# Optimization experiments

Measured on AMD Instinct MI355X. Metric: run time of the kernel, lower is better.

Reference implementation:

```python
import jax, jax.numpy as jnp
import numpy as np

C = 256
NH, NL, NP_ = 8, 3, 4
HD = C // NH
NLAYERS = 6


def sine_pos(H, W, num_feats=128, temperature=10000.0, eps=1e-6):
    # mmdet SinePositionalEncoding with normalize=True and an all-zero padding mask:
    # cumsum of ones -> (i+1), normalized by last element (H or W) * 2*pi.
    scale = 2.0 * np.pi
    y = (jnp.arange(1, H + 1, dtype=jnp.float32) / (H + eps)) * scale
    x = (jnp.arange(1, W + 1, dtype=jnp.float32) / (W + eps)) * scale
    d = jnp.arange(num_feats, dtype=jnp.float32)
    dim_t = temperature ** (2.0 * jnp.floor(d / 2.0) / num_feats)

    def interleave(p):  # p: (n, num_feats) -> sin on even dims, cos on odd dims, interleaved
        return jnp.stack([jnp.sin(p[:, 0::2]), jnp.cos(p[:, 1::2])], axis=-1).reshape(p.shape[0], -1)

    py = interleave(y[:, None] / dim_t)  # (H, num_feats)
    px = interleave(x[:, None] / dim_t)  # (W, num_feats)
    pos = jnp.concatenate([jnp.broadcast_to(py[:, None, :], (H, W, num_feats)),
                           jnp.broadcast_to(px[None, :, :], (H, W, num_feats))], axis=-1)
    return pos.reshape(H * W, 2 * num_feats)


def ref_points(H, W):
    # normalized pixel centers, (x, y) order, shape (H*W, 2)
    ry = (jnp.arange(H, dtype=jnp.float32) + 0.5) / H
    rx = (jnp.arange(W, dtype=jnp.float32) + 0.5) / W
    gy, gx = jnp.meshgrid(ry, rx, indexing='ij')
    return jnp.stack([gx.ravel(), gy.ravel()], axis=-1)


def ln(x, w, b, eps=1e-5):
    m = x.mean(-1, keepdims=True)
    v = x.var(-1, keepdims=True)
    return (x - m) / jnp.sqrt(v + eps) * w + b


def gnorm(x, w, b, groups=32, eps=1e-5):
    B, Ch, H, W = x.shape
    xg = x.reshape(B, groups, Ch // groups, H, W)
    m = xg.mean((2, 3, 4), keepdims=True)
    v = xg.var((2, 3, 4), keepdims=True)
    xg = (xg - m) / jnp.sqrt(v + eps)
    return xg.reshape(B, Ch, H, W) * w[None, :, None, None] + b[None, :, None, None]


def conv3x3(x, w):
    return jax.lax.conv_general_dilated(x, w, (1, 1), 'SAME',
                                        dimension_numbers=('NCHW', 'OIHW', 'NCHW'))


def ms_deform(value, shapes, loc, aw):
    # value (B,S,NH,HD); loc (B,L,NH,NL,NP,2) normalized [0,1]; aw (B,L,NH,NL,NP)
    # Matches F.grid_sample(..., align_corners=False, padding_mode='zeros').
    B, S, nH, hd = value.shape
    Lq, nP = loc.shape[1], loc.shape[4]
    out = jnp.zeros((B, Lq, nH, hd), value.dtype)
    start = 0
    for lvl, (H, W) in enumerate(shapes):
        v = value[:, start:start + H * W].transpose(0, 2, 1, 3)  # (B,nH,HW,hd)
        start += H * W
        l = loc[:, :, :, lvl]                 # (B,Lq,nH,nP,2)
        px = l[..., 0] * W - 0.5
        py = l[..., 1] * H - 0.5
        x0 = jnp.floor(px); y0 = jnp.floor(py)
        lx = px - x0; ly = py - y0
        x0i = x0.astype(jnp.int32); y0i = y0.astype(jnp.int32)

        def tw(w_):  # (B,Lq,nH,nP) -> (B,nH,Lq*nP,1)
            return w_.transpose(0, 2, 1, 3).reshape(B, nH, Lq * nP, 1)

        def gather(xi, yi):
            valid = ((xi >= 0) & (xi < W) & (yi >= 0) & (yi < H)).astype(value.dtype)
            idx = jnp.clip(yi, 0, H - 1) * W + jnp.clip(xi, 0, W - 1)
            idx = idx.transpose(0, 2, 1, 3).reshape(B, nH, Lq * nP)
            g = jnp.take_along_axis(v, idx[..., None], axis=2)  # (B,nH,Lq*nP,hd)
            return g * tw(valid)

        samp = (gather(x0i, y0i) * tw((1 - lx) * (1 - ly))
                + gather(x0i + 1, y0i) * tw(lx * (1 - ly))
                + gather(x0i, y0i + 1) * tw((1 - lx) * ly)
                + gather(x0i + 1, y0i + 1) * tw(lx * ly))
        samp = samp.reshape(B, nH, Lq, nP, hd)
        out = out + jnp.einsum('bqhp,bhqpd->bqhd', aw[:, :, :, lvl], samp)
    return out.reshape(B, Lq, nH * hd)


def _forward(feat0, feat1, feat2, in0_w, in0_b, in1_w, in1_b, in2_w, in2_b,
             off_w, off_b, aw_w, aw_b, vp_w, vp_b, op_w, op_b,
             n1_w, n1_b, ff1_w, ff1_b, ff2_w, ff2_b, n2_w, n2_b,
             fn_w, fn_b, lat_w, lat_b, out_w, gnw, gnb):
    feats = [feat0, feat1, feat2]
    in_ws = [in0_w, in1_w, in2_w]; in_bs = [in0_b, in1_b, in2_b]
    B = feat0.shape[0]
    mlvl = [jnp.einsum('oi,bihw->bohw', w, f) + b[None, :, None, None]
            for f, w, b in zip(feats, in_ws, in_bs)]
    shapes = [(f.shape[2], f.shape[3]) for f in mlvl]
    src = jnp.concatenate([f.reshape(B, C, -1).transpose(0, 2, 1) for f in mlvl], axis=1)  # (B,L,C)
    pos = jnp.concatenate([sine_pos(H, W) for (H, W) in shapes], axis=0)[None]  # (1,L,C)
    ref = jnp.concatenate([ref_points(H, W) for (H, W) in shapes], axis=0)      # (L,2)
    L = ref.shape[0]
    ref = jnp.broadcast_to(ref[None, :, None, :], (B, L, NL, 2))
    norm = jnp.array([[w_, h_] for (h_, w_) in shapes], dtype=src.dtype)  # (NL,2) = (W,H)
    for i in range(NLAYERS):
        q = src + pos
        off = (q @ off_w[i].T + off_b[i]).reshape(B, L, NH, NL, NP_, 2)
        aw = jax.nn.softmax((q @ aw_w[i].T + aw_b[i]).reshape(B, L, NH, NL * NP_), axis=-1)
        aw = aw.reshape(B, L, NH, NL, NP_)
        value = (src @ vp_w[i].T + vp_b[i]).reshape(B, L, NH, HD)
        loc = ref[:, :, None, :, None, :] + off / norm[None, None, None, :, None, :]
        attn = ms_deform(value, shapes, loc, aw) @ op_w[i].T + op_b[i]
        src = ln(src + attn, n1_w[i], n1_b[i])
        ff = jax.nn.relu(src @ ff1_w[i].T + ff1_b[i]) @ ff2_w[i].T + ff2_b[i]
        src = ln(src + ff, n2_w[i], n2_b[i])
    src = ln(src, fn_w, fn_b)
    mems, s = [], 0
    for (H, W) in shapes:
        mems.append(src[:, s:s + H * W].transpose(0, 2, 1).reshape(B, C, H, W))
        s += H * W
    mf = jnp.einsum('oi,bihw->bohw', lat_w, mems[0]) + lat_b[None, :, None, None]
    for i in range(3):
        mf = jax.nn.relu(gnorm(conv3x3(mf, out_w[i]), gnw[i], gnb[i]))
    return (mf, mems[0], mems[1], mems[2])


def setup_inputs():
    ks = iter(jax.random.split(jax.random.key(0), 64))

    def rn(shape, s=0.02):
        return jax.random.normal(next(ks), shape, dtype=jnp.float32) * s

    return dict(
        feat0=rn((1, 256, 64, 64), 1.0),
        feat1=rn((1, 512, 32, 32), 1.0),
        feat2=rn((1, 1024, 16, 16), 1.0),
        in0_w=rn((256, 256)), in0_b=rn((256,)),
        in1_w=rn((256, 512)), in1_b=rn((256,)),
        in2_w=rn((256, 1024)), in2_b=rn((256,)),
        off_w=rn((6, 192, 256), 0.002), off_b=rn((6, 192), 0.5),
        aw_w=rn((6, 96, 256)), aw_b=jnp.zeros((6, 96), jnp.float32),
        vp_w=rn((6, 256, 256)), vp_b=rn((6, 256)),
        op_w=rn((6, 256, 256)), op_b=rn((6, 256)),
        n1_w=jnp.ones((6, 256), jnp.float32), n1_b=jnp.zeros((6, 256), jnp.float32),
        ff1_w=rn((6, 1024, 256)), ff1_b=rn((6, 1024)),
        ff2_w=rn((6, 256, 1024)), ff2_b=rn((6, 256)),
        n2_w=jnp.ones((6, 256), jnp.float32), n2_b=jnp.zeros((6, 256), jnp.float32),
        fn_w=jnp.ones((256,), jnp.float32), fn_b=jnp.zeros((256,), jnp.float32),
        lat_w=rn((256, 256)), lat_b=rn((256,)),
        out_w=rn((3, 256, 256, 3, 3)),
        gnw=jnp.ones((3, 256), jnp.float32), gnb=jnp.zeros((3, 256), jnp.float32),
    )


def reference(feat0, feat1, feat2, in0_w, in0_b, in1_w, in1_b, in2_w, in2_b,
              off_w, off_b, aw_w, aw_b, vp_w, vp_b, op_w, op_b,
              n1_w, n1_b, ff1_w, ff1_b, ff2_w, ff2_b, n2_w, n2_b,
              fn_w, fn_b, lat_w, lat_b, out_w, gnw, gnb):
    return _forward(feat0, feat1, feat2, in0_w, in0_b, in1_w, in1_b, in2_w, in2_b,
                    off_w, off_b, aw_w, aw_b, vp_w, vp_b, op_w, op_b,
                    n1_w, n1_b, ff1_w, ff1_b, ff2_w, ff2_b, n2_w, n2_b,
                    fn_w, fn_b, lat_w, lat_b, out_w, gnw, gnb)
```

## Files before the change

kernel.cpp:

```cpp
#include <hip/hip_runtime.h>
#include <math.h>

#define LTOT 5376

typedef __attribute__((ext_vector_type(8))) __bf16 bf16x8;
typedef __attribute__((ext_vector_type(4))) float f32x4;
typedef __attribute__((ext_vector_type(8))) unsigned short us8;
typedef __attribute__((ext_vector_type(4))) unsigned short us4;

static __device__ __forceinline__ float4 ld4(const float* p) { return *(const float4*)p; }

static __device__ __forceinline__ unsigned short f2bf(float f) {
    unsigned int u = __float_as_uint(f);
    return (unsigned short)((u + 0x7fffu + ((u >> 16) & 1u)) >> 16);
}
static __device__ __forceinline__ float bf2f(unsigned short s) {
    return __uint_as_float(((unsigned int)s) << 16);
}

static __device__ __forceinline__ void gl16(const unsigned short* g, unsigned short* l) {
    __builtin_amdgcn_global_load_lds(
        (const __attribute__((address_space(1))) unsigned int*)g,
        (__attribute__((address_space(3))) unsigned int*)l, 16, 0, 0);
}

__device__ __forceinline__ void gemm_core(
    const unsigned short* __restrict__ A,
    const unsigned short* __restrict__ B,
    const float* __restrict__ bias,
    float* __restrict__ C1, unsigned short* __restrict__ C2,
    const float* __restrict__ posf, unsigned short* __restrict__ qb,
    unsigned short* As, unsigned short* Bs,
    int m0, int mo0, int n0, int N, int K, int omode, int relu)
{
    const int tid  = threadIdx.x;
    const int wave = tid >> 6;
    const int lane = tid & 63;
    const int wm   = (wave >> 1) * 32;
    const int wn   = (wave & 1) * 32;
    const int fr   = lane & 15;
    const int ko   = lane >> 4;

    const int q0 = tid, q1 = tid + 256;
    const int r0 = q0 >> 3, c0v = (q0 & 7) ^ (r0 & 7);
    const int r1 = q1 >> 3, c1v = (q1 & 7) ^ (r1 & 7);
    const unsigned short* a0 = A + (size_t)(m0 + r0) * K + (c0v << 3);
    const unsigned short* a1 = A + (size_t)(m0 + r1) * K + (c1v << 3);
    int bn0 = n0 + r0; if (bn0 > N - 1) bn0 = N - 1;
    int bn1 = n0 + r1; if (bn1 > N - 1) bn1 = N - 1;
    const unsigned short* b0 = B + (size_t)bn0 * K + (c0v << 3);
    const unsigned short* b1 = B + (size_t)bn1 * K + (c1v << 3);
    const int wb = wave << 9;

    f32x4 acc[2][2] = {};
    const int nt = K >> 6;

    auto stage = [&](int buf, int t) {
        const int kof = t << 6;
        gl16(a0 + kof, As + buf * 4096 + wb);
        gl16(a1 + kof, As + buf * 4096 + 2048 + wb);
        gl16(b0 + kof, Bs + buf * 4096 + wb);
        gl16(b1 + kof, Bs + buf * 4096 + 2048 + wb);
    };

    stage(0, 0);
    stage(1, 1);
    asm volatile("s_waitcnt vmcnt(4)" ::: "memory");
    __builtin_amdgcn_s_barrier();
    __builtin_amdgcn_sched_barrier(0);

    for (int t = 0; t < nt; t++) {
        if (t + 2 < nt) stage((t + 2) % 3, t + 2);
        const unsigned short* Ab = As + (t % 3) * 4096;
        const unsigned short* Bb = Bs + (t % 3) * 4096;
        #pragma unroll
        for (int sub = 0; sub < 2; sub++) {
            bf16x8 af[2], bfr[2];
            const int kk = (sub << 2) + ko;
            #pragma unroll
            for (int i = 0; i < 2; i++) {
                int r = wm + i * 16 + fr;
                af[i] = *(const bf16x8*)&Ab[(r << 6) + ((kk ^ (r & 7)) << 3)];
                int c = wn + i * 16 + fr;
                bfr[i] = *(const bf16x8*)&Bb[(c << 6) + ((kk ^ (c & 7)) << 3)];
            }
            #pragma unroll
            for (int i = 0; i < 2; i++)
                #pragma unroll
                for (int j = 0; j < 2; j++)
                    acc[i][j] = __builtin_amdgcn_mfma_f32_16x16x32_bf16(af[i], bfr[j], acc[i][j], 0, 0, 0);
        }
        if (t + 1 < nt) {
            if (t + 2 < nt) asm volatile("s_waitcnt vmcnt(4) lgkmcnt(0)" ::: "memory");
            else            asm volatile("s_waitcnt vmcnt(0) lgkmcnt(0)" ::: "memory");
            __builtin_amdgcn_s_barrier();
            __builtin_amdgcn_sched_barrier(0);
        }
    }

    #pragma unroll
    for (int j = 0; j < 2; j++) {
        int col = n0 + wn + j * 16 + fr;
        if (col >= N) continue;
        float cb = bias[col];
        #pragma unroll
        for (int i = 0; i < 2; i++) {
            #pragma unroll
            for (int r = 0; r < 4; r++) {
                int row = mo0 + wm + i * 16 + ko * 4 + r;
                float v = acc[i][j][r] + cb;
                if (relu) v = fmaxf(v, 0.f);
                size_t off = (size_t)row * N + col;
                if (omode == 0)      C1[off] = v;
                else if (omode == 1) C2[off] = f2bf(v);
                else if (omode == 2) { C1[off] = v; C2[off] = f2bf(v); }
                else { C1[off] = v; C2[off] = f2bf(v); qb[off] = f2bf(v + posf[off]); }
            }
        }
    }
}

__global__ __launch_bounds__(256) void bgemm_k(
    const unsigned short* __restrict__ A, const unsigned short* __restrict__ B,
    const float* __restrict__ bias, float* __restrict__ C1, unsigned short* __restrict__ C2,
    int N, int K, int omode, int relu)
{
    __shared__ unsigned short As[3 * 4096], Bs[3 * 4096];
    int m = blockIdx.y * 64;
    gemm_core(A, B, bias, C1, C2, nullptr, nullptr, As, Bs, m, m, blockIdx.x * 64, N, K, omode, relu);
}

__global__ __launch_bounds__(256) void oavp_k(
    const unsigned short* __restrict__ qbb, const unsigned short* __restrict__ woa,
    const float* __restrict__ boa, float* __restrict__ oab,
    const unsigned short* __restrict__ srcb, const unsigned short* __restrict__ wvp,
    const float* __restrict__ bvp, unsigned short* __restrict__ valb)
{
    __shared__ unsigned short As[3 * 4096], Bs[3 * 4096];
    const int bx = blockIdx.x;
    const int m = blockIdx.y * 64;
    if (bx < 5)
        gemm_core(qbb,  woa, boa, oab, nullptr, nullptr, nullptr, As, Bs, m, m, bx * 64, 288, 256, 0, 0);
    else
        gemm_core(srcb, wvp, bvp, nullptr, valb, nullptr, nullptr, As, Bs, m, m, (bx - 5) * 64, 256, 256, 1, 0);
}

__global__ __launch_bounds__(256) void inproj_k(
    const unsigned short* __restrict__ fT0, const unsigned short* __restrict__ w0, const float* __restrict__ b0,
    const unsigned short* __restrict__ fT1, const unsigned short* __restrict__ w1, const float* __restrict__ b1,
    const unsigned short* __restrict__ fT2, const unsigned short* __restrict__ w2, const float* __restrict__ b2,
    float* __restrict__ src, unsigned short* __restrict__ srcb,
    const float* __restrict__ posf, unsigned short* __restrict__ qbb)
{
    __shared__ unsigned short As[3 * 4096], Bs[3 * 4096];
    const int by = blockIdx.y;
    const int n0 = blockIdx.x * 64;
    if (by < 64)
        gemm_core(fT0, w0, b0, src, srcb, posf, qbb, As, Bs, by * 64, by * 64, n0, 256, 256, 3, 0);
    else if (by < 80)
        gemm_core(fT1, w1, b1, src, srcb, posf, qbb, As, Bs, (by - 64) * 64, 4096 + (by - 64) * 64, n0, 256, 512, 3, 0);
    else
        gemm_core(fT2, w2, b2, src, srcb, posf, qbb, As, Bs, (by - 80) * 64, 5120 + (by - 80) * 64, n0, 256, 1024, 3, 0);
}

__global__ __launch_bounds__(256) void setup_k(
    const float* __restrict__ off_w, const float* __restrict__ off_b,
    const float* __restrict__ aw_w,  const float* __restrict__ aw_b,
    unsigned short* __restrict__ w_oa, float* __restrict__ b_oa,
    const float* __restrict__ out_w, unsigned short* __restrict__ wcb,
    const float* __restrict__ s0, const float* __restrict__ s1,
    const float* __restrict__ s2, const float* __restrict__ s3,
    const float* __restrict__ s4, const float* __restrict__ s5,
    const float* __restrict__ s6, const float* __restrict__ s7,
    unsigned short* __restrict__ dcvt,
    float* __restrict__ pos,
    const float* __restrict__ f0, const float* __restrict__ f1, const float* __restrict__ f2,
    unsigned short* __restrict__ d0, unsigned short* __restrict__ d1, unsigned short* __restrict__ d2)
{
    const int bid = blockIdx.x;
    const int tid = threadIdx.x;
    if (bid < 1728) {
        int idx = bid * 256 + tid;
        int i = idx / 73728;
        int r = idx - i * 73728;
        int n = r >> 8;
        int k = r & 255;
        float v = (n < 192) ? off_w[((size_t)i * 192 + n) * 256 + k]
                            : aw_w[((size_t)i * 96 + (n - 192)) * 256 + k];
        w_oa[idx] = f2bf(v);
        if (k == 0)
            b_oa[i * 288 + n] = (n < 192) ? off_b[i * 192 + n] : aw_b[i * 96 + (n - 192)];
    } else if (bid < 8640) {
        int idx = (bid - 1728) * 256 + tid;
        int c   = idx / 589824;
        int r   = idx - c * 589824;
        int icc = r / 73728;
        int r2  = r - icc * 73728;
        int oc  = r2 / 288;
        int r3  = r2 - oc * 288;
        int tap = r3 >> 5;
        int sl  = r3 & 31;
        int ic  = icc * 32 + (((sl >> 3) ^ ((oc >> 1) & 3)) << 3) + (sl & 7);
        wcb[idx] = f2bf(out_w[(((size_t)(c * 256 + oc)) * 256 + ic) * 9 + tap]);
    } else if (bid < 12992) {
        int i = (bid - 8640) * 256 + tid;
        const float* s; int off;
        if      (i <   98304) { s = s0; off = 0; }
        else if (i <  196608) { s = s1; off = 98304; }
        else if (i <  589824) { s = s2; off = 196608; }
        else if (i <  983040) { s = s3; off = 589824; }
        else if (i <  999424) { s = s4; off = 983040; }
        else if (i < 1032192) { s = s5; off = 999424; }
        else if (i < 1097728) { s = s6; off = 1032192; }
        else                  { s = s7; off = 1097728; }
        float4 v = ld4(&s[(size_t)(i - off) << 2]);
        us4 r = { f2bf(v.x), f2bf(v.y), f2bf(v.z), f2bf(v.w) };
        *(us4*)&dcvt[(size_t)i << 2] = r;
    } else if (bid < 15680) {
        int idx = (bid - 12992) * 256 + tid;
        int l = idx >> 7;
        int pr = idx & 127;
        int half = pr >> 6;
        int j = pr & 63;
        int HW, sh, p;
        if (l < 4096)      { HW = 64; sh = 6; p = l; }
        else if (l < 5120) { HW = 32; sh = 5; p = l - 4096; }
        else               { HW = 16; sh = 4; p = l - 5120; }
        int y = p >> sh;
        int x = p & (HW - 1);
        float invT = exp2f((float)j * (-13.287712379549449f / 64.f));
        float coord = (half == 0) ? (float)(y + 1) : (float)(x + 1);
        float v = coord / ((float)HW + 1e-6f) * 6.283185307179586f;
        float arg = v * invT;
        size_t base = (size_t)l * 256 + half * 128 + (j << 1);
        pos[base]     = sinf(arg);
        pos[base + 1] = cosf(arg);
    } else {
        __shared__ float t[32][33];
        int b = bid - 15680;
        const float* src; unsigned short* dst; int Ci, P, bx, by;
        if (b < 1024)      { src = f0; dst = d0; Ci = 256;  P = 4096; bx = b & 127;        by = b >> 7; }
        else if (b < 1536) { src = f1; dst = d1; Ci = 512;  P = 1024; bx = (b - 1024) & 31; by = (b - 1024) >> 5; }
        else               { src = f2; dst = d2; Ci = 1024; P = 256;  bx = (b - 1536) & 7;  by = (b - 1536) >> 3; }
        int c0 = by * 32, p0 = bx * 32;
        int x = tid & 31, y = tid >> 5;
        for (int i = y; i < 32; i += 8)
            t[i][x] = src[(size_t)(c0 + i) * P + p0 + x];
        __syncthreads();
        for (int i = y; i < 32; i += 8)
            dst[(size_t)(p0 + i) * Ci + c0 + x] = f2bf(t[x][i]);
    }
}

__global__ __launch_bounds__(256) void msdef_k(
    const unsigned short* __restrict__ valb, const float* __restrict__ oab,
    unsigned short* __restrict__ out)
{
    __shared__ float sw[8 * 288];
    const int tid = threadIdx.x;
    const int bl = blockIdx.x;
    #pragma unroll
    for (int id = tid; id < 576; id += 256)
        ((float4*)sw)[id] = ((const float4*)(oab + (size_t)bl * 2304))[id];
    __syncthreads();

    const int p = tid >> 5;
    const int t = tid & 31;
    const int l = bl * 8 + p;
    const int h = t >> 2;
    const int co = (t & 3) << 3;
    const float* mo = sw + p * 288;

    float aw_r[12];
    {
        const float* sc = mo + 192 + h * 12;
        float mx = -1e30f;
        #pragma unroll
        for (int j = 0; j < 12; j++) { aw_r[j] = sc[j]; mx = fmaxf(mx, aw_r[j]); }
        float su = 0.f;
        #pragma unroll
        for (int j = 0; j < 12; j++) { aw_r[j] = expf(aw_r[j] - mx); su += aw_r[j]; }
        float inv = 1.f / su;
        #pragma unroll
        for (int j = 0; j < 12; j++) aw_r[j] *= inv;
    }

    float rx, ry;
    {
        int HW, sh, q;
        if (l < 4096)      { HW = 64; sh = 6; q = l; }
        else if (l < 5120) { HW = 32; sh = 5; q = l - 4096; }
        else               { HW = 16; sh = 4; q = l - 5120; }
        int y = q >> sh;
        int x = q & (HW - 1);
        rx = (x + 0.5f) / (float)HW;
        ry = (y + 0.5f) / (float)HW;
    }

    const int starts[3] = {0, 4096, 5120};
    const int dims[3]   = {64, 32, 16};
    float acc[8] = {};
    #pragma unroll
    for (int s = 0; s < 3; s++) {
        const int D = dims[s];
        const int st = starts[s];
        #pragma unroll
        for (int pt = 0; pt < 4; pt++) {
            float a  = aw_r[(s << 2) + pt];
            float px = rx * D + mo[h * 24 + (s << 3) + (pt << 1)]     - 0.5f;
            float py = ry * D + mo[h * 24 + (s << 3) + (pt << 1) + 1] - 0.5f;
            float x0f = floorf(px), y0f = floorf(py);
            float lx = px - x0f, ly = py - y0f;
            int x0 = (int)x0f, y0 = (int)y0f;
            float w00 = a * (1.f - lx) * (1.f - ly);
            float w10 = a * lx * (1.f - ly);
            float w01 = a * (1.f - lx) * ly;
            float w11 = a * lx * ly;
            #pragma unroll
            for (int cy = 0; cy < 2; cy++) {
                int yi = y0 + cy;
                if (yi < 0 || yi >= D) continue;
                #pragma unroll
                for (int cx = 0; cx < 2; cx++) {
                    int xi = x0 + cx;
                    if (xi < 0 || xi >= D) continue;
                    float w = cy ? (cx ? w11 : w01) : (cx ? w10 : w00);
                    us8 v = *(const us8*)&valb[((size_t)(st + yi * D + xi) << 8) + (h << 5) + co];
                    #pragma unroll
                    for (int e = 0; e < 8; e++)
                        acc[e] = fmaf(w, bf2f(v[e]), acc[e]);
                }
            }
        }
    }
    us8 r;
    #pragma unroll
    for (int e = 0; e < 8; e++) r[e] = f2bf(acc[e]);
    *(us8*)&out[((size_t)l << 8) + (h << 5) + co] = r;
}

template<bool HAS_POS>
__global__ __launch_bounds__(256) void ln_k(float* __restrict__ src, const float* __restrict__ add,
                                            const float* __restrict__ w, const float* __restrict__ b,
                                            unsigned short* __restrict__ outb,
                                            const float* __restrict__ posf,
                                            unsigned short* __restrict__ qbout)
{
    int row = blockIdx.x * 4 + (threadIdx.x >> 6);
    int lane = threadIdx.x & 63;
    size_t base = (size_t)row * 256 + (lane << 2);
    float4 x = ld4(&src[base]);
    float4 a = ld4(&add[base]);
    x.x += a.x; x.y += a.y; x.z += a.z; x.w += a.w;
    float s = x.x + x.y + x.z + x.w;
    #pragma unroll
    for (int o = 32; o > 0; o >>= 1) s += __shfl_xor(s, o, 64);
    float m = s * (1.f / 256.f);
    float d0 = x.x - m, d1 = x.y - m, d2 = x.z - m, d3 = x.w - m;
    float v = d0 * d0 + d1 * d1 + d2 * d2 + d3 * d3;
    #pragma unroll
    for (int o = 32; o > 0; o >>= 1) v += __shfl_xor(v, o, 64);
    float rs = rsqrtf(v * (1.f / 256.f) + 1e-5f);
    float4 wv = ld4(&w[lane << 2]);
    float4 bv = ld4(&b[lane << 2]);
    float4 o4;
    o4.x = d0 * rs * wv.x + bv.x;
    o4.y = d1 * rs * wv.y + bv.y;
    o4.z = d2 * rs * wv.z + bv.z;
    o4.w = d3 * rs * wv.w + bv.w;
    *(float4*)&src[base] = o4;
    us4 r = { f2bf(o4.x), f2bf(o4.y), f2bf(o4.z), f2bf(o4.w) };
    *(us4*)&outb[base] = r;
    if (HAS_POS) {
        float4 p4 = ld4(&posf[base]);
        us4 q = { f2bf(o4.x + p4.x), f2bf(o4.y + p4.y), f2bf(o4.z + p4.z), f2bf(o4.w + p4.w) };
        *(us4*)&qbout[base] = q;
    }
}

__global__ __launch_bounds__(256) void ln2fn_k(float* __restrict__ src, const float* __restrict__ add,
                                               const float* __restrict__ w2, const float* __restrict__ b2,
                                               const float* __restrict__ wf, const float* __restrict__ bf,
                                               unsigned short* __restrict__ outb)
{
    int row = blockIdx.x * 4 + (threadIdx.x >> 6);
    int lane = threadIdx.x & 63;
    size_t base = (size_t)row * 256 + (lane << 2);
    float4 x = ld4(&src[base]);
    float4 a = ld4(&add[base]);
    x.x += a.x; x.y += a.y; x.z += a.z; x.w += a.w;
    float s = x.x + x.y + x.z + x.w;
    #pragma unroll
    for (int o = 32; o > 0; o >>= 1) s += __shfl_xor(s, o, 64);
    float m = s * (1.f / 256.f);
    float d0 = x.x - m, d1 = x.y - m, d2 = x.z - m, d3 = x.w - m;
    float v = d0 * d0 + d1 * d1 + d2 * d2 + d3 * d3;
    #pragma unroll
    for (int o = 32; o > 0; o >>= 1) v += __shfl_xor(v, o, 64);
    float rs = rsqrtf(v * (1.f / 256.f) + 1e-5f);
    float4 wv = ld4(&w2[lane << 2]);
    float4 bv = ld4(&b2[lane << 2]);
    float4 o4;
    o4.x = d0 * rs * wv.x + bv.x;
    o4.y = d1 * rs * wv.y + bv.y;
    o4.z = d2 * rs * wv.z + bv.z;
    o4.w = d3 * rs * wv.w + bv.w;
    float s2 = o4.x + o4.y + o4.z + o4.w;
    #pragma unroll
    for (int o = 32; o > 0; o >>= 1) s2 += __shfl_xor(s2, o, 64);
    float m2 = s2 * (1.f / 256.f);
    float e0 = o4.x - m2, e1 = o4.y - m2, e2 = o4.z - m2, e3 = o4.w - m2;
    float v2 = e0 * e0 + e1 * e1 + e2 * e2 + e3 * e3;
    #pragma unroll
    for (int o = 32; o > 0; o >>= 1) v2 += __shfl_xor(v2, o, 64);
    float rs2 = rsqrtf(v2 * (1.f / 256.f) + 1e-5f);
    float4 wf4 = ld4(&wf[lane << 2]);
    float4 bf4 = ld4(&bf[lane << 2]);
    float4 o5;
    o5.x = e0 * rs2 * wf4.x + bf4.x;
    o5.y = e1 * rs2 * wf4.y + bf4.y;
    o5.z = e2 * rs2 * wf4.z + bf4.z;
    o5.w = e3 * rs2 * wf4.w + bf4.w;
    *(float4*)&src[base] = o5;
    us4 r = { f2bf(o5.x), f2bf(o5.y), f2bf(o5.z), f2bf(o5.w) };
    *(us4*)&outb[base] = r;
}

__global__ __launch_bounds__(256) void tail_k(
    const float* __restrict__ src, float* __restrict__ outb_,
    const unsigned short* __restrict__ srcb, const unsigned short* __restrict__ w_lat,
    const float* __restrict__ lat_b, unsigned short* __restrict__ latb)
{
    if (blockIdx.x < 1344) {
        __shared__ float t[32][33];
        int b = blockIdx.x;
        int bx = b % 168, cy = b / 168;
        const float* s; float* d; int HW, p0;
        if (bx < 128)      { s = src;           d = outb_;           HW = 4096; p0 = bx * 32; }
        else if (bx < 160) { s = src + 1048576; d = outb_ + 1048576; HW = 1024; p0 = (bx - 128) * 32; }
        else               { s = src + 1310720; d = outb_ + 1310720; HW = 256;  p0 = (bx - 160) * 32; }
        int c0 = cy * 32;
        int x = threadIdx.x & 31, y = threadIdx.x >> 5;
        for (int i = y; i < 32; i += 8)
            t[i][x] = s[(size_t)(p0 + i) * 256 + c0 + x];
        __syncthreads();
        for (int i = y; i < 32; i += 8)
            d[(size_t)(c0 + i) * HW + p0 + x] = t[x][i];
    } else {
        __shared__ unsigned short As[3 * 4096], Bs[3 * 4096];
        int b = blockIdx.x - 1344;
        int m = (b >> 2) * 64;
        gemm_core(srcb, w_lat, lat_b, nullptr, latb, nullptr, nullptr, As, Bs,
                  m, m, (b & 3) * 64, 256, 256, 1, 0);
    }
}

__global__ __launch_bounds__(256) void conv3b_k(const unsigned short* __restrict__ inb,
                                                const unsigned short* __restrict__ wcb,
                                                float* __restrict__ out)
{
    __shared__ __align__(16) unsigned char smem[25344];
    unsigned short* sIn = (unsigned short*)smem;
    unsigned short* sW  = (unsigned short*)(smem + 6912);
    float* sO = (float*)smem;

    const int tid = threadIdx.x;
    const int mb = blockIdx.x;
    const int y0 = (mb >> 2) << 2;
    const int x0 = (mb & 3) << 4;
    const int oc0 = blockIdx.y << 5;
    const int wave = tid >> 6, lane = tid & 63;
    const int wm = (wave >> 1) * 32;
    const int wn = (wave & 1) * 16;
    const int fr = lane & 15, ko = lane >> 4;

    f32x4 acc[2] = {};

    for (int icc = 0; icc < 8; icc++) {
        __syncthreads();
        #pragma unroll
        for (int id = tid; id < 432; id += 256) {
            int pxi = id >> 2, ch = id & 3;
            int r = pxi / 18, s = pxi - r * 18;
            int gy = y0 - 1 + r, gx = x0 - 1 + s;
            us8 v = {};
            if (gy >= 0 && gy < 64 && gx >= 0 && gx < 64)
                v = *(const us8*)&inb[((size_t)(gy * 64 + gx) << 8) + (icc << 5) + (ch << 3)];
            *(us8*)&sIn[(pxi << 5) + ((ch ^ ((s >> 1) & 3)) << 3)] = v;
        }
        const unsigned short* wsrc = wcb + (((size_t)icc * 256 + oc0) * 9 << 5);
        #pragma unroll
        for (int id = tid; id < 1152; id += 256)
            *(us8*)&sW[id << 3] = *(const us8*)&wsrc[id << 3];
        __syncthreads();

        #pragma unroll
        for (int tap = 0; tap < 9; tap++) {
            const int ky = tap / 3, kx = tap - ky * 3;
            bf16x8 a[2], b;
            #pragma unroll
            for (int i = 0; i < 2; i++) {
                int px = wm + i * 16 + fr;
                int r = (px >> 4) + ky;
                int s = (px & 15) + kx;
                a[i] = *(const bf16x8*)&sIn[(((r * 18 + s)) << 5) + ((ko ^ ((s >> 1) & 3)) << 3)];
            }
            {
                int oc = wn + fr;
                b = *(const bf16x8*)&sW[(((oc * 9) + tap) << 5) + ((ko ^ ((oc >> 1) & 3)) << 3)];
            }
            #pragma unroll
            for (int i = 0; i < 2; i++)
                acc[i] = __builtin_amdgcn_mfma_f32_16x16x32_bf16(a[i], b, acc[i], 0, 0, 0);
        }
    }

    __syncthreads();
    #pragma unroll
    for (int i = 0; i < 2; i++) {
        int oc = wn + fr;
        int pxb = wm + i * 16 + ko * 4;
        *(f32x4*)&sO[oc * 68 + pxb] = acc[i];
    }
    __syncthreads();
    {
        int oc_r = tid >> 3;
        int yy   = (tid >> 1) & 3;
        int xh   = (tid & 1) << 3;
        float* dst = &out[(size_t)(oc0 + oc_r) * 4096 + (y0 + yy) * 64 + x0 + xh];
        const float* srcl = &sO[oc_r * 68 + yy * 16 + xh];
        *(float4*)&dst[0] = *(const float4*)&srcl[0];
        *(float4*)&dst[4] = *(const float4*)&srcl[4];
    }
}

template<int OUT>
__global__ __launch_bounds__(1024) void gn_k(const float* __restrict__ x,
                                             const float* __restrict__ w, const float* __restrict__ b,
                                             unsigned short* __restrict__ ob, float* __restrict__ of)
{
    const int g = blockIdx.x;
    const float* p = x + (size_t)g * 32768;
    float s = 0.f, ss = 0.f;
    for (int i = threadIdx.x * 4; i < 32768; i += 4096) {
        float4 v = ld4(&p[i]);
        s  += v.x + v.y + v.z + v.w;
        ss += v.x * v.x + v.y * v.y + v.z * v.z + v.w * v.w;
    }
    #pragma unroll
    for (int o = 32; o > 0; o >>= 1) {
        s  += __shfl_xor(s, o, 64);
        ss += __shfl_xor(ss, o, 64);
    }
    __shared__ float rs[16], rss[16];
    int wid = threadIdx.x >> 6;
    if ((threadIdx.x & 63) == 0) { rs[wid] = s; rss[wid] = ss; }
    __syncthreads();
    float S = 0.f, SS = 0.f;
    #pragma unroll
    for (int k = 0; k < 16; k++) { S += rs[k]; SS += rss[k]; }
    float m = S * (1.f / 32768.f);
    float rstd = rsqrtf(SS * (1.f / 32768.f) - m * m + 1e-5f);

    for (int i = threadIdx.x; i < 8192; i += 1024) {
        int cl = i >> 10;
        int c = (g << 3) + cl;
        float sw = w[c], sb = b[c];
        float4 v = ld4(&p[(size_t)i << 2]);
        float r0 = fmaxf((v.x - m) * rstd * sw + sb, 0.f);
        float r1 = fmaxf((v.y - m) * rstd * sw + sb, 0.f);
        float r2 = fmaxf((v.z - m) * rstd * sw + sb, 0.f);
        float r3 = fmaxf((v.w - m) * rstd * sw + sb, 0.f);
        if (OUT == 0) {
            int px0 = (i & 1023) << 2;
            ob[(size_t)(px0 + 0) * 256 + c] = f2bf(r0);
            ob[(size_t)(px0 + 1) * 256 + c] = f2bf(r1);
            ob[(size_t)(px0 + 2) * 256 + c] = f2bf(r2);
            ob[(size_t)(px0 + 3) * 256 + c] = f2bf(r3);
        } else {
            float4 r = make_float4(r0, r1, r2, r3);
            *(float4*)&of[(size_t)g * 32768 + ((size_t)i << 2)] = r;
        }
    }
}

extern "C" void kernel_launch(void* const* d_in, const int* in_sizes, int n_in,
                              void* d_out, int out_size, void* d_ws, size_t ws_size,
                              hipStream_t stream)
{
    (void)in_sizes; (void)n_in; (void)out_size; (void)ws_size;
    const float* feat0 = (const float*)d_in[0];
    const float* feat1 = (const float*)d_in[1];
    const float* feat2 = (const float*)d_in[2];
    const float* in0_w = (const float*)d_in[3];
    const float* in0_b = (const float*)d_in[4];
    const float* in1_w = (const float*)d_in[5];
    const float* in1_b = (const float*)d_in[6];
    const float* in2_w = (const float*)d_in[7];
    const float* in2_b = (const float*)d_in[8];
    const float* off_w = (const float*)d_in[9];
    const float* off_b = (const float*)d_in[10];
    const float* aw_w  = (const float*)d_in[11];
    const float* aw_b  = (const float*)d_in[12];
    const float* vp_w  = (const float*)d_in[13];
    const float* vp_b  = (const float*)d_in[14];
    const float* op_w  = (const float*)d_in[15];
    const float* op_b  = (const float*)d_in[16];
    const float* n1_w  = (const float*)d_in[17];
    const float* n1_b  = (const float*)d_in[18];
    const float* ff1_w = (const float*)d_in[19];
    const float* ff1_b = (const float*)d_in[20];
    const float* ff2_w = (const float*)d_in[21];
    const float* ff2_b = (const float*)d_in[22];
    const float* n2_w  = (const float*)d_in[23];
    const float* n2_b  = (const float*)d_in[24];
    const float* fn_w  = (const float*)d_in[25];
    const float* fn_b  = (const float*)d_in[26];
    const float* lat_w = (const float*)d_in[27];
    const float* lat_b = (const float*)d_in[28];
    const float* out_w = (const float*)d_in[29];
    const float* gnw   = (const float*)d_in[30];
    const float* gnb   = (const float*)d_in[31];
    float* out = (float*)d_out;

    float* ws     = (float*)d_ws;
    float* src    = ws;
    float* pos    = src  + 1376256;
    float* tmp    = pos  + 1376256;
    float* valbuf = tmp  + 1376256;
    float* oab    = valbuf + 1376256;
    float* stats  = oab  + 1548288;
    float* boa    = stats + 64;
    float* pong   = pos;

    unsigned short* valb = (unsigned short*)valbuf;
    unsigned short* latb = (unsigned short*)(valbuf + 688128);

    unsigned short* ub = (unsigned short*)(boa + 1728);
    unsigned short* srcb  = ub; ub += 1376256;
    unsigned short* qbb   = ub; ub += 1376256;
    unsigned short* msdb  = ub; ub += 1376256;
    unsigned short* ffhb  = ub; ub += 5505024;
    unsigned short* w_oa  = ub; ub += 442368;
    unsigned short* w_vp  = ub; ub += 393216;
    unsigned short* w_op  = ub; ub += 393216;
    unsigned short* w_ff1 = ub; ub += 1572864;
    unsigned short* w_ff2 = ub; ub += 1572864;
    unsigned short* w_in0 = ub; ub += 65536;
    unsigned short* w_in1 = ub; ub += 131072;
    unsigned short* w_in2 = ub; ub += 262144;
    unsigned short* w_lat = ub; ub += 65536;
    unsigned short* wcb   = ub; ub += 1769472;

    unsigned short* fT0 = ffhb;
    unsigned short* fT1 = ffhb + 1048576;
    unsigned short* fT2 = ffhb + 1572864;
    unsigned short* pingb = qbb;

    setup_k<<<17472, 256, 0, stream>>>(off_w, off_b, aw_w, aw_b, w_oa, boa,
                                       out_w, wcb,
                                       vp_w, op_w, ff1_w, ff2_w, in0_w, in1_w, in2_w, lat_w, w_vp,
                                       pos,
                                       feat0, feat1, feat2, fT0, fT1, fT2);

    inproj_k<<<dim3(4, 84), 256, 0, stream>>>(fT0, w_in0, in0_b, fT1, w_in1, in1_b,
                                              fT2, w_in2, in2_b, src, srcb, pos, qbb);

    for (int i = 0; i < 6; i++) {
        oavp_k<<<dim3(9, 84), 256, 0, stream>>>(qbb, w_oa + i*73728, boa + i*288, oab,
                                                srcb, w_vp + i*65536, vp_b + i*256, valb);
        msdef_k<<<672, 256, 0, stream>>>(valb, oab, msdb);
        bgemm_k<<<dim3(4, 84), 256, 0, stream>>>(msdb, w_op + i*65536, op_b + i*256, tmp, nullptr, 256, 256, 0, 0);
        ln_k<false><<<1344, 256, 0, stream>>>(src, tmp, n1_w + i*256, n1_b + i*256, srcb, nullptr, nullptr);
        bgemm_k<<<dim3(16, 84), 256, 0, stream>>>(srcb, w_ff1 + i*262144, ff1_b + i*1024, nullptr, ffhb, 1024, 256, 1, 1);
        bgemm_k<<<dim3(4, 84), 256, 0, stream>>>(ffhb, w_ff2 + i*262144, ff2_b + i*256, tmp, nullptr, 256, 1024, 0, 0);
        if (i < 5)
            ln_k<true><<<1344, 256, 0, stream>>>(src, tmp, n2_w + i*256, n2_b + i*256, srcb, pos, qbb);
        else
            ln2fn_k<<<1344, 256, 0, stream>>>(src, tmp, n2_w + i*256, n2_b + i*256, fn_w, fn_b, srcb);
    }

    tail_k<<<1600, 256, 0, stream>>>(src, out + 1048576, srcb, w_lat, lat_b, latb);

    conv3b_k<<<dim3(64, 8), 256, 0, stream>>>(latb, wcb, pong);
    gn_k<0><<<32, 1024, 0, stream>>>(pong, gnw, gnb, pingb, nullptr);

    conv3b_k<<<dim3(64, 8), 256, 0, stream>>>(pingb, wcb + 589824, pong);
    gn_k<0><<<32, 1024, 0, stream>>>(pong, gnw + 256, gnb + 256, pingb, nullptr);

    conv3b_k<<<dim3(64, 8), 256, 0, stream>>>(pingb, wcb + 1179648, pong);
    gn_k<1><<<32, 1024, 0, stream>>>(pong, gnw + 512, gnb + 512, nullptr, out);
}
```

Measured before the change: 606.0 us.

## Fuse LayerNorms into following GEMM prologues for FFN1 and offset/value projections

Removes the standalone LayerNorm kernels. Each consumer GEMM block now recomputes the residual add and LayerNorm for its 64-row tile directly into shared memory as the bf16 A operand. Only the K loop over the B matrix is pipelined, and one column block writes back the fp32 residual stream, which moves to a new ysrc buffer. This saves two launches per layer and the bf16 round trips through global memory. In exchange, every column block redoes the LayerNorm: 16 blocks per row tile for FFN1 and 9 for oavp. It also computes variance as E[x²]−m² instead of the two-pass form.

```diff
diff --git a/kernel.cpp b/kernel.cpp
--- a/kernel.cpp
+++ b/kernel.cpp
@@ -161,6 +161,185 @@
         gemm_core(fT1, w1, b1, src, srcb, posf, qbb, As, Bs, (by - 64) * 64, 4096 + (by - 64) * 64, n0, 256, 512, 3, 0);
     else
         gemm_core(fT2, w2, b2, src, srcb, posf, qbb, As, Bs, (by - 80) * 64, 5120 + (by - 80) * 64, n0, 256, 1024, 3, 0);
+}
+
+__device__ __forceinline__ void ln_stage(
+    const float* __restrict__ X, const float* __restrict__ R,
+    const float* __restrict__ lnw, const float* __restrict__ lnb,
+    const float* __restrict__ posf, float* __restrict__ wout,
+    unsigned short* As, int m0)
+{
+    const int t = threadIdx.x;
+    const int r = t >> 2;
+    const int q = t & 3;
+    const size_t base = (size_t)(m0 + r) * 256 + (q << 6);
+    float4 xv[16];
+    float s = 0.f, ss = 0.f;
+    #pragma unroll
+    for (int k = 0; k < 16; k++) {
+        float4 a = ld4(&X[base + (k << 2)]);
+        float4 b = ld4(&R[base + (k << 2)]);
+        a.x += b.x; a.y += b.y; a.z += b.z; a.w += b.w;
+        xv[k] = a;
+        s  += a.x + a.y + a.z + a.w;
+        ss += a.x * a.x + a.y * a.y + a.z * a.z + a.w * a.w;
+    }
+    #pragma unroll
+    for (int o = 1; o < 4; o <<= 1) {
+        s  += __shfl_xor(s,  o, 64);
+        ss += __shfl_xor(ss, o, 64);
+    }
+    float m = s * (1.f / 256.f);
+    float rstd = rsqrtf(ss * (1.f / 256.f) - m * m + 1e-5f);
+    #pragma unroll
+    for (int k = 0; k < 16; k++) {
+        int c = (q << 6) + (k << 2);
+        float4 w4 = ld4(&lnw[c]);
+        float4 b4 = ld4(&lnb[c]);
+        float4 o;
+        o.x = (xv[k].x - m) * rstd * w4.x + b4.x;
+        o.y = (xv[k].y - m) * rstd * w4.y + b4.y;
+        o.z = (xv[k].z - m) * rstd * w4.z + b4.z;
+        o.w = (xv[k].w - m) * rstd * w4.w + b4.w;
+        xv[k] = o;
+    }
+    if (wout) {
+        #pragma unroll
+        for (int k = 0; k < 16; k++)
+            *(float4*)&wout[base + (k << 2)] = xv[k];
+    }
+    if (posf) {
+        #pragma unroll
+        for (int k = 0; k < 16; k++) {
+            float4 p = ld4(&posf[base + (k << 2)]);
+            xv[k].x += p.x; xv[k].y += p.y; xv[k].z += p.z; xv[k].w += p.w;
+        }
+    }
+    #pragma unroll
+    for (int j = 0; j < 8; j++) {
+        float4 lo = xv[2 * j], hi = xv[2 * j + 1];
+        us8 v = { f2bf(lo.x), f2bf(lo.y), f2bf(lo.z), f2bf(lo.w),
+                  f2bf(hi.x), f2bf(hi.y), f2bf(hi.z), f2bf(hi.w) };
+        int c8 = (q << 3) + j;
+        int slot = (c8 & 24) | ((c8 ^ (r & 7)) & 7);
+        *(us8*)&As[(r << 8) + (slot << 3)] = v;
+    }
+}
+
+__device__ __forceinline__ void gemm_afix(
+    const unsigned short* __restrict__ B, const float* __restrict__ bias,
+    float* __restrict__ C1, unsigned short* __restrict__ C2,
+    const unsigned short* As, unsigned short* Bs,
+    int m0, int n0, int N, int omode, int relu)
+{
+    const int tid = threadIdx.x;
+    const int wave = tid >> 6, lane = tid & 63;
+    const int wm = (wave >> 1) * 32, wn = (wave & 1) * 32;
+    const int fr = lane & 15, ko = lane >> 4;
+
+    const int q0 = tid, q1 = tid + 256;
+    const int r0 = q0 >> 3, c0v = (q0 & 7) ^ (r0 & 7);
+    const int r1 = q1 >> 3, c1v = (q1 & 7) ^ (r1 & 7);
+    int bn0 = n0 + r0; if (bn0 > N - 1) bn0 = N - 1;
+    int bn1 = n0 + r1; if (bn1 > N - 1) bn1 = N - 1;
+    const unsigned short* b0 = B + (size_t)bn0 * 256 + (c0v << 3);
+    const unsigned short* b1 = B + (size_t)bn1 * 256 + (c1v << 3);
+    const int wb = wave << 9;
+
+    f32x4 acc[2][2] = {};
+
+    auto stage = [&](int buf, int t) {
+        const int kof = t << 6;
+        gl16(b0 + kof, Bs + buf * 4096 + wb);
+        gl16(b1 + kof, Bs + buf * 4096 + 2048 + wb);
+    };
+
+    stage(0, 0);
+    stage(1, 1);
+    asm volatile("s_waitcnt vmcnt(2) lgkmcnt(0)" ::: "memory");
+    __builtin_amdgcn_s_barrier();
+    __builtin_amdgcn_sched_barrier(0);
+
+    for (int t = 0; t < 4; t++) {
+        if (t + 2 < 4) stage((t + 2) % 3, t + 2);
+        const unsigned short* Bb = Bs + (t % 3) * 4096;
+        #pragma unroll
+        for (int sub = 0; sub < 2; sub++) {
+            const int kk = (sub << 2) + ko;
+            const int kg = (t << 3) + kk;
+            bf16x8 af[2], bfr[2];
+            #pragma unroll
+            for (int i = 0; i < 2; i++) {
+                int rr = wm + i * 16 + fr;
+                int slot = (kg & 24) | ((kg ^ (rr & 7)) & 7);
+                af[i] = *(const bf16x8*)&As[(rr << 8) + (slot << 3)];
+                int cc = wn + i * 16 + fr;
+                bfr[i] = *(const bf16x8*)&Bb[(cc << 6) + ((kk ^ (cc & 7)) << 3)];
+            }
+            #pragma unroll
+            for (int i = 0; i < 2; i++)
+                #pragma unroll
+                for (int j = 0; j < 2; j++)
+                    acc[i][j] = __builtin_amdgcn_mfma_f32_16x16x32_bf16(af[i], bfr[j], acc[i][j], 0, 0, 0);
+        }
+        if (t + 1 < 4) {
+            if (t + 2 < 4) asm volatile("s_waitcnt vmcnt(2) lgkmcnt(0)" ::: "memory");
+            else           asm volatile("s_waitcnt vmcnt(0) lgkmcnt(0)" ::: "memory");
+            __builtin_amdgcn_s_barrier();
+            __builtin_amdgcn_sched_barrier(0);
+        }
+    }
+
+    #pragma unroll
+    for (int j = 0; j < 2; j++) {
+        int col = n0 + wn + j * 16 + fr;
+        if (col >= N) continue;
+        float cb = bias[col];
+        #pragma unroll
+        for (int i = 0; i < 2; i++) {
+            #pragma unroll
+            for (int r = 0; r < 4; r++) {
+                int row = m0 + wm + i * 16 + ko * 4 + r;
+                float v = acc[i][j][r] + cb;
+                if (relu) v = fmaxf(v, 0.f);
+                size_t off = (size_t)row * N + col;
+                if (omode == 0) C1[off] = v;
+                else            C2[off] = f2bf(v);
+            }
+        }
+    }
+}
+
+__global__ __launch_bounds__(256) void ffln_k(
+    const float* __restrict__ X, const float* __restrict__ R,
+    const float* __restrict__ lnw, const float* __restrict__ lnb,
+    const unsigned short* __restrict__ B, const float* __restrict__ bias,
+    unsigned short* __restrict__ C2, float* __restrict__ Yout)
+{
+    __shared__ __align__(16) unsigned short As[16384];
+    __shared__ __align__(16) unsigned short Bs[12288];
+    const int m0 = blockIdx.y << 6;
+    ln_stage(X, R, lnw, lnb, nullptr, (blockIdx.x == 0) ? Yout : nullptr, As, m0);
+    gemm_afix(B, bias, nullptr, C2, As, Bs, m0, blockIdx.x << 6, 1024, 1, 1);
+}
+
+__global__ __launch_bounds__(256) void oavpln_k(
+    const float* __restrict__ X, const float* __restrict__ R,
+    const float* __restrict__ lnw, const float* __restrict__ lnb,
+    const float* __restrict__ posf,
+    const unsigned short* __restrict__ Boa, const float* __restrict__ boa, float* __restrict__ oab,
+    const unsigned short* __restrict__ Bvp, const float* __restrict__ bvp, unsigned short* __restrict__ valb,
+    float* __restrict__ Xout)
+{
+    __shared__ __align__(16) unsigned short As[16384];
+    __shared__ __align__(16) unsigned short Bs[12288];
+    const int bx = blockIdx.x;
+    const int m0 = blockIdx.y << 6;
+    ln_stage(X, R, lnw, lnb, (bx < 5) ? posf : nullptr, (bx == 0) ? Xout : nullptr, As, m0);
+    if (bx < 5)
+        gemm_afix(Boa, boa, oab, nullptr, As, Bs, m0, bx << 6, 288, 0, 0);
+    else
+        gemm_afix(Bvp, bvp, nullptr, valb, As, Bs, m0, (bx - 5) << 6, 256, 1, 0);
 }
 
 __global__ __launch_bounds__(256) void setup_k(
@@ -339,45 +518,6 @@
     *(us8*)&out[((size_t)l << 8) + (h << 5) + co] = r;
 }
 
-template<bool HAS_POS>
-__global__ __launch_bounds__(256) void ln_k(float* __restrict__ src, const float* __restrict__ add,
-                                            const float* __restrict__ w, const float* __restrict__ b,
-                                            unsigned short* __restrict__ outb,
-                                            const float* __restrict__ posf,
-                                            unsigned short* __restrict__ qbout)
-{
-    int row = blockIdx.x * 4 + (threadIdx.x >> 6);
-    int lane = threadIdx.x & 63;
-    size_t base = (size_t)row * 256 + (lane << 2);
-    float4 x = ld4(&src[base]);
-    float4 a = ld4(&add[base]);
-    x.x += a.x; x.y += a.y; x.z += a.z; x.w += a.w;
-    float s = x.x + x.y + x.z + x.w;
-    #pragma unroll
-    for (int o = 32; o > 0; o >>= 1) s += __shfl_xor(s, o, 64);
-    float m = s * (1.f / 256.f);
-    float d0 = x.x - m, d1 = x.y - m, d2 = x.z - m, d3 = x.w - m;
-    float v = d0 * d0 + d1 * d1 + d2 * d2 + d3 * d3;
-    #pragma unroll
-    for (int o = 32; o > 0; o >>= 1) v += __shfl_xor(v, o, 64);
-    float rs = rsqrtf(v * (1.f / 256.f) + 1e-5f);
-    float4 wv = ld4(&w[lane << 2]);
-    float4 bv = ld4(&b[lane << 2]);
-    float4 o4;
-    o4.x = d0 * rs * wv.x + bv.x;
-    o4.y = d1 * rs * wv.y + bv.y;
-    o4.z = d2 * rs * wv.z + bv.z;
-    o4.w = d3 * rs * wv.w + bv.w;
-    *(float4*)&src[base] = o4;
-    us4 r = { f2bf(o4.x), f2bf(o4.y), f2bf(o4.z), f2bf(o4.w) };
-    *(us4*)&outb[base] = r;
-    if (HAS_POS) {
-        float4 p4 = ld4(&posf[base]);
-        us4 q = { f2bf(o4.x + p4.x), f2bf(o4.y + p4.y), f2bf(o4.z + p4.z), f2bf(o4.w + p4.w) };
-        *(us4*)&qbout[base] = q;
-    }
-}
-
 __global__ __launch_bounds__(256) void ln2fn_k(float* __restrict__ src, const float* __restrict__ add,
                                                const float* __restrict__ w2, const float* __restrict__ b2,
                                                const float* __restrict__ wf, const float* __restrict__ bf,
@@ -631,12 +771,13 @@
     float* oab    = valbuf + 1376256;
     float* stats  = oab  + 1548288;
     float* boa    = stats + 64;
+    float* ysrc   = boa  + 1728;
     float* pong   = pos;
 
     unsigned short* valb = (unsigned short*)valbuf;
     unsigned short* latb = (unsigned short*)(valbuf + 688128);
 
-    unsigned short* ub = (unsigned short*)(boa + 1728);
+    unsigned short* ub = (unsigned short*)(ysrc + 1376256);
     unsigned short* srcb  = ub; ub += 1376256;
     unsigned short* qbb   = ub; ub += 1376256;
     unsigned short* msdb  = ub; ub += 1376256;
@@ -667,20 +808,27 @@
                                               fT2, w_in2, in2_b, src, srcb, pos, qbb);
 
     for (int i = 0; i < 6; i++) {
-        oavp_k<<<dim3(9, 84), 256, 0, stream>>>(qbb, w_oa + i*73728, boa + i*288, oab,
-                                                srcb, w_vp + i*65536, vp_b + i*256, valb);
+        if (i == 0)
+            oavp_k<<<dim3(9, 84), 256, 0, stream>>>(qbb, w_oa, boa, oab,
+                                                    srcb, w_vp, vp_b, valb);
+        else
+            oavpln_k<<<dim3(9, 84), 256, 0, stream>>>(ysrc, tmp,
+                                                      n2_w + (i - 1) * 256, n2_b + (i - 1) * 256, pos,
+                                                      w_oa + i * 73728, boa + i * 288, oab,
+                                                      w_vp + i * 65536, vp_b + i * 256, valb,
+                                                      src);
         msdef_k<<<672, 256, 0, stream>>>(valb, oab, msdb);
-        bgemm_k<<<dim3(4, 84), 256, 0, stream>>>(msdb, w_op + i*65536, op_b + i*256, tmp, nullptr, 256, 256, 0, 0);
-        ln_k<false><<<1344, 256, 0, stream>>>(src, tmp, n1_w + i*256, n1_b + i*256, srcb, nullptr, nullptr);
-        bgemm_k<<<dim3(16, 84), 256, 0, stream>>>(srcb, w_ff1 + i*262144, ff1_b + i*1024, nullptr, ffhb, 1024, 256, 1, 1);
-        bgemm_k<<<dim3(4, 84), 256, 0, stream>>>(ffhb, w_ff2 + i*262144, ff2_b + i*256, tmp, nullptr, 256, 1024, 0, 0);
-        if (i < 5)
-            ln_k<true><<<1344, 256, 0, stream>>>(src, tmp, n2_w + i*256, n2_b + i*256, srcb, pos, qbb);
-        else
-            ln2fn_k<<<1344, 256, 0, stream>>>(src, tmp, n2_w + i*256, n2_b + i*256, fn_w, fn_b, srcb);
-    }
-
-    tail_k<<<1600, 256, 0, stream>>>(src, out + 1048576, srcb, w_lat, lat_b, latb);
+        bgemm_k<<<dim3(4, 84), 256, 0, stream>>>(msdb, w_op + i * 65536, op_b + i * 256,
+                                                 tmp, nullptr, 256, 256, 0, 0);
+        ffln_k<<<dim3(16, 84), 256, 0, stream>>>(src, tmp, n1_w + i * 256, n1_b + i * 256,
+                                                 w_ff1 + i * 262144, ff1_b + i * 1024,
+                                                 ffhb, ysrc);
+        bgemm_k<<<dim3(4, 84), 256, 0, stream>>>(ffhb, w_ff2 + i * 262144, ff2_b + i * 256,
+                                                 tmp, nullptr, 256, 1024, 0, 0);
+    }
+    ln2fn_k<<<1344, 256, 0, stream>>>(ysrc, tmp, n2_w + 5 * 256, n2_b + 5 * 256, fn_w, fn_b, srcb);
+
+    tail_k<<<1600, 256, 0, stream>>>(ysrc, out + 1048576, srcb, w_lat, lat_b, latb);
 
     conv3b_k<<<dim3(64, 8), 256, 0, stream>>>(latb, wcb, pong);
     gn_k<0><<<32, 1024, 0, stream>>>(pong, gnw, gnb, pingb, nullptr);
```

Measured after the change: 1.052 ms. 73.6% more time.
